# Kernel optimization log

Measured on AMD Instinct MI355X. Metric: run time of the kernel, lower is better.

Reference implementation:

```python
import jax, jax.numpy as jnp
import numpy as np

DIM = 20
N = 200000
E = 6400000
ITERATIONS = 3


def setup_inputs() -> dict:
    key = jax.random.key(0)
    ks = jax.random.split(key, 20)
    inp = {
        "h": jax.random.normal(ks[0], (N, DIM), dtype=jnp.float32),
        "node2depth": jax.random.randint(ks[1], (N,), 0, 5, dtype=jnp.int32),
        "edge_src": jax.random.randint(ks[2], (E,), 0, N, dtype=jnp.int32),
        "edge_dst": jax.random.randint(ks[3], (E,), 0, N, dtype=jnp.int32),
    }
    # Six DIM x DIM Linear layers (weight stored [out,in] like torch, plus bias)
    scale = 1.0 / np.sqrt(DIM)
    names = ["Wz", "Uz", "Wr", "Ur", "Wh", "Uh"]
    for j, nm in enumerate(names):
        inp[nm + "_w"] = jax.random.uniform(ks[4 + 2 * j], (DIM, DIM), jnp.float32, -scale, scale)
        inp[nm + "_b"] = jax.random.uniform(ks[5 + 2 * j], (DIM,), jnp.float32, -scale, scale)
    return inp


def _linear(x, w, b):
    return x @ w.T + b


def reference(h, Wz_w, Wz_b, Uz_w, Uz_b, Wr_w, Wr_b, Ur_w, Ur_b,
              Wh_w, Wh_b, Uh_w, Uh_b, node2depth, edge_src, edge_dst):
    active = None
    for i in range(ITERATIONS):
        # active set shrinks as i grows (depth + i <= ITERATIONS)
        active = (node2depth + i) <= ITERATIONS  # [N] bool
        af = active.astype(h.dtype)
        # x[u] = sum over neighbors v of h[v], counting only active src AND active dst
        msg = h[edge_src] * af[edge_src][:, None]          # [E, DIM]
        x = jax.ops.segment_sum(msg, edge_dst, num_segments=N)  # [N, DIM]
        x = x * af[:, None]
        z = jax.nn.sigmoid(_linear(x, Wz_w, Wz_b) + _linear(h, Uz_w, Uz_b))
        r = jax.nn.sigmoid(_linear(x, Wr_w, Wr_b) + _linear(h, Ur_w, Ur_b))
        h_cand = jnp.tanh(_linear(x, Wh_w, Wh_b) + _linear(r * h, Uh_w, Uh_b))
        h_new = z * h + (1.0 - z) * h_cand
        # inactive nodes are dropped from the dict in the original; since the
        # active set only shrinks, keeping their old h is equivalent
        h = jnp.where(active[:, None], h_new, h)
    # original returns only nodes active at the last iteration; zero out the rest
    return jnp.where(active[:, None], h, jnp.zeros_like(h))
```

## Files before the change

kernel.cpp:

```cpp
#include <hip/hip_runtime.h>

#define DIM    20
#define NN     200000
#define EE     6400000
#define ITERS  3
#define BLOCK  256

#define NODES_PER_FINE   64
#define NFINE            3125
#define NCOARSE          98
#define FINE_PER_COARSE  32

#define TILE1            2048
#define IPT1             8

#define TILE             4096
#define IPT              16

#define CAP1             57344
#define NT2P             14
#define CAP2             2048
#define PIPT             8

#define XSTRIDE          21

typedef unsigned int u32;

__device__ __forceinline__ u32 pack_bf16x2(float a, float b) {
    u32 ua = __float_as_uint(a);
    u32 ub = __float_as_uint(b);
    ua = (ua + 0x7FFFu + ((ua >> 16) & 1u)) >> 16;
    ub = (ub + 0x7FFFu + ((ub >> 16) & 1u)) & 0xFFFF0000u;
    return ua | ub;
}

__global__ __launch_bounds__(BLOCK) void setup(const float* __restrict__ h,
                                               const int* __restrict__ depth,
                                               u32* __restrict__ hbA,
                                               u32* __restrict__ hbC,
                                               u32* __restrict__ CT,
                                               int* __restrict__ coarse_cursor,
                                               int* __restrict__ fine_cursor,
                                               int* __restrict__ gcur) {
    int g = blockIdx.x * BLOCK + threadIdx.x;
    if (g < NCOARSE) coarse_cursor[g] = g * CAP1;
    if (g < NFINE)   fine_cursor[g]   = g * CAP2;
    if (g == 0) *gcur = 0;
    if (g < NN / 8) {
        int4 a = *(const int4*)(depth + g * 8);
        int4 b = *(const int4*)(depth + g * 8 + 4);
        CT[g] = ((u32)a.x & 7u)        | (((u32)a.y & 7u) << 4)
              | (((u32)a.z & 7u) << 8) | (((u32)a.w & 7u) << 12)
              | (((u32)b.x & 7u) << 16)| (((u32)b.y & 7u) << 20)
              | (((u32)b.z & 7u) << 24)| (((u32)b.w & 7u) << 28);
    }
    int node = g >> 3, s = g & 7;
    if (depth[node] > ITERS) return;
    float2 f = *(const float2*)(h + (size_t)node * DIM + s * 2);
    hbA[(size_t)node * 8 + s] = pack_bf16x2(f.x, f.y);
    if (s < 2) {
        float2 fc = *(const float2*)(h + (size_t)node * DIM + 16 + s * 2);
        hbC[(size_t)node * 2 + s] = pack_bf16x2(fc.x, fc.y);
    }
}

__global__ __launch_bounds__(BLOCK) void p1_split(const int* __restrict__ esrc,
                                                  const int* __restrict__ edst,
                                                  const u32* __restrict__ CT,
                                                  int* __restrict__ coarse_cursor,
                                                  u32* __restrict__ buf1) {
    __shared__ u32 hist[NCOARSE];
    __shared__ u32 lbase[NCOARSE];
    __shared__ u32 gbase[NCOARSE];
    __shared__ u32 lout[TILE1];
    int tid = threadIdx.x;
    int start = blockIdx.x * TILE1;
    if (tid < NCOARSE) hist[tid] = 0;
    __syncthreads();

    int4 d4[2], s4[2];
    #pragma unroll
    for (int q = 0; q < 2; ++q) {
        int e4 = start + (q * BLOCK + tid) * 4;
        d4[q] = *(const int4*)(edst + e4);
        s4[q] = *(const int4*)(esrc + e4);
    }
    int dd[IPT1], ss[IPT1];
    dd[0]=d4[0].x; dd[1]=d4[0].y; dd[2]=d4[0].z; dd[3]=d4[0].w;
    dd[4]=d4[1].x; dd[5]=d4[1].y; dd[6]=d4[1].z; dd[7]=d4[1].w;
    ss[0]=s4[0].x; ss[1]=s4[0].y; ss[2]=s4[0].z; ss[3]=s4[0].w;
    ss[4]=s4[1].x; ss[5]=s4[1].y; ss[6]=s4[1].z; ss[7]=s4[1].w;

    u32 cls[IPT1];
    #pragma unroll
    for (int k = 0; k < IPT1; ++k)
        cls[k] = (CT[(u32)ss[k] >> 3] >> (((u32)ss[k] & 7u) << 2)) & 7u;
    asm volatile("" :: "v"(cls[0]), "v"(cls[1]), "v"(cls[2]), "v"(cls[3]),
                       "v"(cls[4]), "v"(cls[5]), "v"(cls[6]), "v"(cls[7]));

    u32 rank[IPT1];
    #pragma unroll
    for (int k = 0; k < IPT1; ++k)
        if (cls[k] <= 3u) rank[k] = atomicAdd(&hist[(u32)dd[k] >> 11], 1u);
    __syncthreads();

    if (tid < 64) {
        u32 a = hist[tid];
        u32 b = (tid + 64 < NCOARSE) ? hist[tid + 64] : 0u;
        u32 ia = a, ib = b;
        #pragma unroll
        for (int off = 1; off < 64; off <<= 1) {
            u32 ta = (u32)__shfl_up((int)ia, off, 64);
            u32 tb = (u32)__shfl_up((int)ib, off, 64);
            if (tid >= off) { ia += ta; ib += tb; }
        }
        u32 totA = (u32)__shfl((int)ia, 63, 64);
        lbase[tid] = ia - a;
        if (tid + 64 < NCOARSE) lbase[tid + 64] = totA + ib - b;
    }
    __syncthreads();
    if (tid < NCOARSE) {
        u32 cq = hist[tid];
        gbase[tid] = cq ? (u32)atomicAdd((u32*)&coarse_cursor[tid], cq) : 0u;
    }
    #pragma unroll
    for (int k = 0; k < IPT1; ++k)
        if (cls[k] <= 3u)
            lout[lbase[(u32)dd[k] >> 11] + rank[k]] =
                ((u32)dd[k] & 2047u) | ((u32)ss[k] << 11) | (cls[k] << 29);
    __syncthreads();
    int wid = tid >> 6, lane = tid & 63;
    for (int b = wid; b < NCOARSE; b += 4) {
        u32 cq = hist[b], lb = lbase[b], gb = gbase[b];
        for (u32 i = lane; i < cq; i += 64)
            buf1[gb + i] = lout[lb + i];
    }
}

__global__ __launch_bounds__(BLOCK) void p2_split(const u32* __restrict__ buf1,
                                                  const int* __restrict__ coarse_cursor,
                                                  int* __restrict__ fine_cursor,
                                                  u32* __restrict__ buf2) {
    int bid = blockIdx.x;
    int c = bid / NT2P, t = bid - c * NT2P;
    int base  = c * CAP1;
    int end   = coarse_cursor[c];
    int start = base + t * TILE;
    if (start >= end) return;

    __shared__ u32 hist[FINE_PER_COARSE];
    __shared__ u32 lbase[FINE_PER_COARSE];
    __shared__ u32 gbase[FINE_PER_COARSE];
    __shared__ u32 lout[TILE];
    int tid = threadIdx.x;
    if (tid < FINE_PER_COARSE) hist[tid] = 0;
    __syncthreads();

    u32 w[IPT];
    #pragma unroll
    for (int q = 0; q < 4; ++q) {
        int i4 = start + (q * BLOCK + tid) * 4;
        if (i4 + 3 < end) {
            uint4 v = *(const uint4*)(buf1 + i4);
            w[q * 4 + 0] = v.x; w[q * 4 + 1] = v.y;
            w[q * 4 + 2] = v.z; w[q * 4 + 3] = v.w;
        } else {
            #pragma unroll
            for (int j = 0; j < 4; ++j) {
                int i = i4 + j;
                w[q * 4 + j] = (i < end) ? buf1[i] : 0xFFFFFFFFu;
            }
        }
    }
    u32 rank[IPT];
    #pragma unroll
    for (int k = 0; k < IPT; ++k)
        if (w[k] != 0xFFFFFFFFu)
            rank[k] = atomicAdd(&hist[(w[k] & 2047u) >> 6], 1u);
    __syncthreads();

    if (tid < 32) {
        u32 a = hist[tid], ia = a;
        #pragma unroll
        for (int off = 1; off < 32; off <<= 1) {
            u32 ta = (u32)__shfl_up((int)ia, off, 32);
            if (tid >= off) ia += ta;
        }
        lbase[tid] = ia - a;
        int f = c * FINE_PER_COARSE + tid;
        gbase[tid] = a ? (u32)atomicAdd((u32*)&fine_cursor[f], a) : 0u;
    }
    __syncthreads();
    #pragma unroll
    for (int k = 0; k < IPT; ++k)
        if (w[k] != 0xFFFFFFFFu)
            lout[lbase[(w[k] & 2047u) >> 6] + rank[k]] = (w[k] & 63u) | ((w[k] >> 11) << 6);
    __syncthreads();
    int wid = tid >> 6, lane = tid & 63;
    for (int b = wid; b < FINE_PER_COARSE; b += 4) {
        u32 cq = hist[b], lb = lbase[b], gb = gbase[b];
        for (u32 i = lane; i < cq; i += 64)
            buf2[gb + i] = lout[lb + i];
    }
}


__device__ __forceinline__ float bl(u32 w) { return __uint_as_float(w << 16); }
__device__ __forceinline__ float bh(u32 w) { return __uint_as_float(w & 0xFFFF0000u); }

__device__ __forceinline__ void acc_half(float* xa, float* xc, uint4 a, u32 c) {
    xa[0]+=bl(a.x); xa[1]+=bh(a.x);
    xa[2]+=bl(a.y); xa[3]+=bh(a.y);
    xa[4]+=bl(a.z); xa[5]+=bh(a.z);
    xa[6]+=bl(a.w); xa[7]+=bh(a.w);
    xc[0]+=bl(c);   xc[1]+=bh(c);
}

__device__ __forceinline__ float fast_sigmoid(float t) {
    return 1.0f / (1.0f + __expf(-t));
}
__device__ __forceinline__ float fast_tanh(float t) {
    t = fminf(fmaxf(t, -15.0f), 15.0f);
    float e2 = __expf(2.0f * t);
    return (e2 - 1.0f) / (e2 + 1.0f);
}

__device__ __forceinline__ void gru_body(
    int u, int tid, const float* xl,
    const float* __restrict__ h_in, float* __restrict__ h_out,
    u32* __restrict__ hbA_out, u32* __restrict__ hbC_out,
    int du, int limNext, int isFinal,
    const float* __restrict__ Wz, const float* __restrict__ bWz,
    const float* __restrict__ Uz, const float* __restrict__ bUz,
    const float* __restrict__ Wr, const float* __restrict__ bWr,
    const float* __restrict__ Ur, const float* __restrict__ bUr,
    const float* __restrict__ Wh, const float* __restrict__ bWh,
    const float* __restrict__ Uh, const float* __restrict__ bUh)
{
    float x[DIM], h[DIM];
    #pragma unroll
    for (int k = 0; k < DIM; ++k) x[k] = xl[tid * XSTRIDE + k];
    {
        const float4* hv = (const float4*)(h_in + (size_t)u * DIM);
        float4 a0 = hv[0], a1 = hv[1], a2 = hv[2], a3 = hv[3], a4 = hv[4];
        h[0]=a0.x; h[1]=a0.y; h[2]=a0.z; h[3]=a0.w;
        h[4]=a1.x; h[5]=a1.y; h[6]=a1.z; h[7]=a1.w;
        h[8]=a2.x; h[9]=a2.y; h[10]=a2.z; h[11]=a2.w;
        h[12]=a3.x; h[13]=a3.y; h[14]=a3.z; h[15]=a3.w;
        h[16]=a4.x; h[17]=a4.y; h[18]=a4.z; h[19]=a4.w;
    }

    float z[DIM], rh[DIM];
    #pragma unroll
    for (int j = 0; j < DIM; ++j) {
        float sz = bWz[j] + bUz[j];
        float sr = bWr[j] + bUr[j];
        #pragma unroll
        for (int k = 0; k < DIM; ++k) {
            sz += x[k] * Wz[j * DIM + k];
            sz += h[k] * Uz[j * DIM + k];
            sr += x[k] * Wr[j * DIM + k];
            sr += h[k] * Ur[j * DIM + k];
        }
        z[j]  = fast_sigmoid(sz);
        rh[j] = fast_sigmoid(sr) * h[j];
    }

    float o[DIM];
    #pragma unroll
    for (int j = 0; j < DIM; ++j) {
        float sh = bWh[j] + bUh[j];
        #pragma unroll
        for (int k = 0; k < DIM; ++k) {
            sh += x[k]  * Wh[j * DIM + k];
            sh += rh[k] * Uh[j * DIM + k];
        }
        float hc = fast_tanh(sh);
        o[j] = z[j] * h[j] + (1.0f - z[j]) * hc;
    }

    {
        float4* o4 = (float4*)(h_out + (size_t)u * DIM);
        o4[0] = make_float4(o[0],  o[1],  o[2],  o[3]);
        o4[1] = make_float4(o[4],  o[5],  o[6],  o[7]);
        o4[2] = make_float4(o[8],  o[9],  o[10], o[11]);
        o4[3] = make_float4(o[12], o[13], o[14], o[15]);
        o4[4] = make_float4(o[16], o[17], o[18], o[19]);
    }
    if (!isFinal && du <= limNext) {
        u32* rowA = hbA_out + (size_t)u * 8;
        uint4 wA0 = make_uint4(pack_bf16x2(o[0], o[1]),   pack_bf16x2(o[2], o[3]),
                               pack_bf16x2(o[4], o[5]),   pack_bf16x2(o[6], o[7]));
        uint4 wA1 = make_uint4(pack_bf16x2(o[8], o[9]),   pack_bf16x2(o[10], o[11]),
                               pack_bf16x2(o[12], o[13]), pack_bf16x2(o[14], o[15]));
        *(uint4*)rowA       = wA0;
        *(uint4*)(rowA + 4) = wA1;
        *(uint2*)(hbC_out + (size_t)u * 2) =
            make_uint2(pack_bf16x2(o[16], o[17]), pack_bf16x2(o[18], o[19]));
    }
}

__global__ __launch_bounds__(BLOCK) void pb_gru(
    const u32* __restrict__ buf2, const int* __restrict__ fine_cursor,
    int* __restrict__ gcur,
    int* __restrict__ ptr, u32* __restrict__ cnt3, u32* __restrict__ ssrc,
    const u32* __restrict__ hbA_in, const u32* __restrict__ hbC_in,
    u32* __restrict__ hbA_out, u32* __restrict__ hbC_out,
    const float* __restrict__ h_in, float* __restrict__ h_out,
    const int* __restrict__ depth,
    const float* __restrict__ Wz, const float* __restrict__ bWz,
    const float* __restrict__ Uz, const float* __restrict__ bUz,
    const float* __restrict__ Wr, const float* __restrict__ bWr,
    const float* __restrict__ Ur, const float* __restrict__ bUr,
    const float* __restrict__ Wh, const float* __restrict__ bWh,
    const float* __restrict__ Uh, const float* __restrict__ bUh)
{
    __shared__ u32 hist[512];
    __shared__ u32 ebase[512];
    __shared__ u32 lout[CAP2];
    __shared__ u32 wsum[4];
    __shared__ int slo;
    __shared__ float xl[64 * XSTRIDE];
    int tid = threadIdx.x;
    int f = blockIdx.x;
    int base = f * CAP2;
    int end  = fine_cursor[f];
    int cnt  = end - base;
    hist[tid] = 0; hist[tid + 256] = 0;
    __syncthreads();

    u32 w[PIPT];
    #pragma unroll
    for (int q = 0; q < 2; ++q) {
        int i4 = base + (q * BLOCK + tid) * 4;
        if (i4 + 3 < end) {
            uint4 v = *(const uint4*)(buf2 + i4);
            w[q * 4 + 0] = v.x; w[q * 4 + 1] = v.y;
            w[q * 4 + 2] = v.z; w[q * 4 + 3] = v.w;
        } else {
            #pragma unroll
            for (int j = 0; j < 4; ++j) {
                int i = i4 + j;
                w[q * 4 + j] = (i < end) ? buf2[i] : 0xFFFFFFFFu;
            }
        }
    }
    u32 key[PIPT], rank[PIPT];
    #pragma unroll
    for (int k = 0; k < PIPT; ++k) {
        if (w[k] != 0xFFFFFFFFu) {
            u32 cls = (w[k] >> 24) & 7u;
            key[k]  = (w[k] & 63u) * 8u + cls;
            rank[k] = atomicAdd(&hist[key[k]], 1u);
        }
    }
    if (tid == 0) slo = atomicAdd(gcur, cnt);
    __syncthreads();
    {
        u32 s0 = hist[2 * tid], s1 = hist[2 * tid + 1];
        u32 s = s0 + s1;
        int lane = tid & 63, wid = tid >> 6;
        u32 incl = s;
        #pragma unroll
        for (int off = 1; off < 64; off <<= 1) {
            u32 t = __shfl_up((int)incl, off, 64);
            if (lane >= off) incl += t;
        }
        if (lane == 63) wsum[wid] = incl;
        __syncthreads();
        u32 woff = 0;
        for (int w2 = 0; w2 < wid; ++w2) woff += wsum[w2];
        u32 excl = woff + incl - s;
        ebase[2 * tid]     = excl;
        ebase[2 * tid + 1] = excl + s0;
    }
    __syncthreads();
    int lo = slo;
    if (tid < NODES_PER_FINE) {
        u32 base0 = ebase[tid * 8];
        u32 cc1 = ebase[tid * 8 + 2] - base0;
        u32 cc2 = ebase[tid * 8 + 3] - base0;
        u32 cc3 = ebase[tid * 8 + 4] - base0;
        int u = f * NODES_PER_FINE + tid;
        ptr[u]  = lo + (int)base0;
        cnt3[u] = cc1 | (cc2 << 10) | (cc3 << 20);
    }
    #pragma unroll
    for (int k = 0; k < PIPT; ++k) {
        if (w[k] != 0xFFFFFFFFu) lout[ebase[key[k]] + rank[k]] = (w[k] >> 6) & 0x3FFFFu;
    }
    __syncthreads();
    for (int j = tid; j < cnt; j += BLOCK) ssrc[lo + j] = lout[j];

    int t = tid & 7, team = tid >> 3;
    int r = t >> 1, q = t & 1;
    #pragma unroll
    for (int rep = 0; rep < 2; ++rep) {
        int nl = team + rep * 32;
        int u = f * NODES_PER_FINE + nl;
        if (depth[u] <= ITERS) {
            int b0 = (int)ebase[nl * 8];
            int d  = (int)(ebase[nl * 8 + 4] - ebase[nl * 8]);

            float xa[8], xc[2];
            #pragma unroll
            for (int k = 0; k < 8; ++k) xa[k] = 0.0f;
            xc[0] = 0.0f; xc[1] = 0.0f;

            int e = r;
            for (; e + 12 < d; e += 16) {
                u32 p0 = lout[b0 + e];
                u32 p1 = lout[b0 + e + 4];
                u32 p2 = lout[b0 + e + 8];
                u32 p3 = lout[b0 + e + 12];
                uint4 a0 = *(const uint4*)(hbA_in + (size_t)p0 * 8 + q * 4);
                uint4 a1 = *(const uint4*)(hbA_in + (size_t)p1 * 8 + q * 4);
                uint4 a2 = *(const uint4*)(hbA_in + (size_t)p2 * 8 + q * 4);
                uint4 a3 = *(const uint4*)(hbA_in + (size_t)p3 * 8 + q * 4);
                u32 cc0 = hbC_in[(size_t)p0 * 2 + q];
                u32 cc1 = hbC_in[(size_t)p1 * 2 + q];
                u32 cc2 = hbC_in[(size_t)p2 * 2 + q];
                u32 cc3 = hbC_in[(size_t)p3 * 2 + q];
                acc_half(xa, xc, a0, cc0);
                acc_half(xa, xc, a1, cc1);
                acc_half(xa, xc, a2, cc2);
                acc_half(xa, xc, a3, cc3);
            }
            for (; e + 4 < d; e += 8) {
                u32 p0 = lout[b0 + e];
                u32 p1 = lout[b0 + e + 4];
                uint4 a0 = *(const uint4*)(hbA_in + (size_t)p0 * 8 + q * 4);
                uint4 a1 = *(const uint4*)(hbA_in + (size_t)p1 * 8 + q * 4);
                u32 cc0 = hbC_in[(size_t)p0 * 2 + q];
                u32 cc1 = hbC_in[(size_t)p1 * 2 + q];
                acc_half(xa, xc, a0, cc0);
                acc_half(xa, xc, a1, cc1);
            }
            if (e < d) {
                u32 p0 = lout[b0 + e];
                uint4 a0 = *(const uint4*)(hbA_in + (size_t)p0 * 8 + q * 4);
                u32 cc0 = hbC_in[(size_t)p0 * 2 + q];
                acc_half(xa, xc, a0, cc0);
            }
            #pragma unroll
            for (int k = 0; k < 8; ++k) {
                xa[k] += __shfl_xor(xa[k], 2, 64);
                xa[k] += __shfl_xor(xa[k], 4, 64);
            }
            xc[0] += __shfl_xor(xc[0], 2, 64); xc[0] += __shfl_xor(xc[0], 4, 64);
            xc[1] += __shfl_xor(xc[1], 2, 64); xc[1] += __shfl_xor(xc[1], 4, 64);

            float* xr = xl + nl * XSTRIDE;
            if (t == 0) {
                #pragma unroll
                for (int k = 0; k < 8; ++k) xr[k] = xa[k];
                xr[16] = xc[0]; xr[17] = xc[1];
            } else if (t == 1) {
                #pragma unroll
                for (int k = 0; k < 8; ++k) xr[8 + k] = xa[k];
                xr[18] = xc[0]; xr[19] = xc[1];
            }
        }
    }
    __syncthreads();
    if (tid >= 64) return;

    int u = f * NODES_PER_FINE + tid;
    int du = depth[u];
    if (du > ITERS) return;
    gru_body(u, tid, xl, h_in, h_out, hbA_out, hbC_out, du, 2, 0,
             Wz, bWz, Uz, bUz, Wr, bWr, Ur, bUr, Wh, bWh, Uh, bUh);
}


__global__ __launch_bounds__(BLOCK) void grnn_iter(
    const u32* __restrict__ hbA_in, const u32* __restrict__ hbC_in,
    u32* __restrict__ hbA_out, u32* __restrict__ hbC_out,
    const float* __restrict__ h_in, float* __restrict__ h_out,
    const int* __restrict__ depth, const int* __restrict__ ptr,
    const u32* __restrict__ cnt3, const u32* __restrict__ ssrc,
    const float* __restrict__ Wz, const float* __restrict__ bWz,
    const float* __restrict__ Uz, const float* __restrict__ bUz,
    const float* __restrict__ Wr, const float* __restrict__ bWr,
    const float* __restrict__ Ur, const float* __restrict__ bUr,
    const float* __restrict__ Wh, const float* __restrict__ bWh,
    const float* __restrict__ Uh, const float* __restrict__ bUh,
    int lim, int limNext, int shift, int isFinal)
{
    __shared__ float xl[64 * XSTRIDE];
    int tid = threadIdx.x;
    int t = tid & 7, team = tid >> 3;
    int r = t >> 1, q = t & 1;

    #pragma unroll
    for (int rep = 0; rep < 2; ++rep) {
        int nl = team + rep * 32;
        int u = blockIdx.x * 64 + nl;
        if (depth[u] <= lim) {
            int p = ptr[u];
            int d = (int)((cnt3[u] >> shift) & 1023u);

            float xa[8], xc[2];
            #pragma unroll
            for (int k = 0; k < 8; ++k) xa[k] = 0.0f;
            xc[0] = 0.0f; xc[1] = 0.0f;

            int e = r;
            for (; e + 12 < d; e += 16) {
                u32 p0 = ssrc[p + e];
                u32 p1 = ssrc[p + e + 4];
                u32 p2 = ssrc[p + e + 8];
                u32 p3 = ssrc[p + e + 12];
                uint4 a0 = *(const uint4*)(hbA_in + (size_t)p0 * 8 + q * 4);
                uint4 a1 = *(const uint4*)(hbA_in + (size_t)p1 * 8 + q * 4);
                uint4 a2 = *(const uint4*)(hbA_in + (size_t)p2 * 8 + q * 4);
                uint4 a3 = *(const uint4*)(hbA_in + (size_t)p3 * 8 + q * 4);
                u32 cc0 = hbC_in[(size_t)p0 * 2 + q];
                u32 cc1 = hbC_in[(size_t)p1 * 2 + q];
                u32 cc2 = hbC_in[(size_t)p2 * 2 + q];
                u32 cc3 = hbC_in[(size_t)p3 * 2 + q];
                acc_half(xa, xc, a0, cc0);
                acc_half(xa, xc, a1, cc1);
                acc_half(xa, xc, a2, cc2);
                acc_half(xa, xc, a3, cc3);
            }
            for (; e + 4 < d; e += 8) {
                u32 p0 = ssrc[p + e];
                u32 p1 = ssrc[p + e + 4];
                uint4 a0 = *(const uint4*)(hbA_in + (size_t)p0 * 8 + q * 4);
                uint4 a1 = *(const uint4*)(hbA_in + (size_t)p1 * 8 + q * 4);
                u32 cc0 = hbC_in[(size_t)p0 * 2 + q];
                u32 cc1 = hbC_in[(size_t)p1 * 2 + q];
                acc_half(xa, xc, a0, cc0);
                acc_half(xa, xc, a1, cc1);
            }
            if (e < d) {
                u32 p0 = ssrc[p + e];
                uint4 a0 = *(const uint4*)(hbA_in + (size_t)p0 * 8 + q * 4);
                u32 cc0 = hbC_in[(size_t)p0 * 2 + q];
                acc_half(xa, xc, a0, cc0);
            }
            #pragma unroll
            for (int k = 0; k < 8; ++k) {
                xa[k] += __shfl_xor(xa[k], 2, 64);
                xa[k] += __shfl_xor(xa[k], 4, 64);
            }
            xc[0] += __shfl_xor(xc[0], 2, 64); xc[0] += __shfl_xor(xc[0], 4, 64);
            xc[1] += __shfl_xor(xc[1], 2, 64); xc[1] += __shfl_xor(xc[1], 4, 64);

            float* xr = xl + nl * XSTRIDE;
            if (t == 0) {
                #pragma unroll
                for (int k = 0; k < 8; ++k) xr[k] = xa[k];
                xr[16] = xc[0]; xr[17] = xc[1];
            } else if (t == 1) {
                #pragma unroll
                for (int k = 0; k < 8; ++k) xr[8 + k] = xa[k];
                xr[18] = xc[0]; xr[19] = xc[1];
            }
        }
    }
    __syncthreads();
    if (tid >= 64) return;

    int u = blockIdx.x * 64 + tid;
    int du = depth[u];
    if (du > lim) {
        if (isFinal) {
            float4 z4 = make_float4(0.f, 0.f, 0.f, 0.f);
            float4* o4 = (float4*)(h_out + (size_t)u * DIM);
            #pragma unroll
            for (int qq = 0; qq < 5; ++qq) o4[qq] = z4;
        }
        return;
    }
    gru_body(u, tid, xl, h_in, h_out, hbA_out, hbC_out, du, limNext, isFinal,
             Wz, bWz, Uz, bUz, Wr, bWr, Ur, bUr, Wh, bWh, Uh, bUh);
}


extern "C" void kernel_launch(void* const* d_in, const int* in_sizes, int n_in,
                              void* d_out, int out_size, void* d_ws, size_t ws_size,
                              hipStream_t stream) {
    const float* h0    = (const float*)d_in[0];
    const int*   depth = (const int*)d_in[1];
    const int*   esrc  = (const int*)d_in[2];
    const int*   edst  = (const int*)d_in[3];
    const float* Wz  = (const float*)d_in[4];  const float* bWz = (const float*)d_in[5];
    const float* Uz  = (const float*)d_in[6];  const float* bUz = (const float*)d_in[7];
    const float* Wr  = (const float*)d_in[8];  const float* bWr = (const float*)d_in[9];
    const float* Ur  = (const float*)d_in[10]; const float* bUr = (const float*)d_in[11];
    const float* Wh  = (const float*)d_in[12]; const float* bWh = (const float*)d_in[13];
    const float* Uh  = (const float*)d_in[14]; const float* bUh = (const float*)d_in[15];
    float* out = (float*)d_out;

    int* W = (int*)d_ws;
    u32*  CT            = (u32*)(W + 0);
    int*  gcur          = W + 25024;
    int*  coarse_cursor = W + 25088;
    int*  fine_cursor   = W + 25216;
    int*  ptr           = W + 28416;
    u32*  cnt3          = (u32*)(W + 228416);
    u32*  buf1          = (u32*)(W + 428416);
    u32*  buf2          = buf1 + (size_t)NCOARSE * CAP1;
    float* h1           = (float*)(buf2 + (size_t)NFINE * CAP2);
    u32*  hbA0          = (u32*)(h1 + (size_t)NN * DIM);
    u32*  hbC0          = hbA0 + (size_t)NN * 8;
    u32*  hbA1          = hbC0 + (size_t)NN * 2;
    u32*  hbC1          = hbA1 + (size_t)NN * 8;
    u32*  ssrc          = buf1;

    setup   <<<(NN * 8) / BLOCK, BLOCK, 0, stream>>>(h0, depth, hbA0, hbC0, CT,
                                                     coarse_cursor, fine_cursor, gcur);
    p1_split<<<EE / TILE1, BLOCK, 0, stream>>>(esrc, edst, CT, coarse_cursor, buf1);
    p2_split<<<NCOARSE * NT2P, BLOCK, 0, stream>>>(buf1, coarse_cursor, fine_cursor, buf2);

    pb_gru  <<<NFINE, BLOCK, 0, stream>>>(buf2, fine_cursor, gcur, ptr, cnt3, ssrc,
        hbA0, hbC0, hbA1, hbC1, h0, h1, depth,
        Wz, bWz, Uz, bUz, Wr, bWr, Ur, bUr, Wh, bWh, Uh, bUh);

    grnn_iter<<<NN / 64, BLOCK, 0, stream>>>(hbA1, hbC1, hbA0, hbC0, h1, h1,
        depth, ptr, cnt3, ssrc,
        Wz, bWz, Uz, bUz, Wr, bWr, Ur, bUr, Wh, bWh, Uh, bUh, 2, 1, 10, 0);
    grnn_iter<<<NN / 64, BLOCK, 0, stream>>>(hbA0, hbC0, hbA1, hbC1, h1, out,
        depth, ptr, cnt3, ssrc,
        Wz, bWz, Uz, bUz, Wr, bWr, Ur, bUr, Wh, bWh, Uh, bUh, 1, 0, 0, 1);
}
```

Baseline: 485.1 us.

## Sort fused-kernel gather edges by source-id bucket for locality

In the fused partition+GRU kernel, a second LDS histogram and counting sort orders each destination node's edges by a 2-bit bucket of the source id (bits 22-23 of the packed word). The two node-teams per thread group then interleave their gathers chunk by chunk, so concurrent loads across the block hit a narrower range of source rows and get better L2/MALL locality. The cost is extra LDS (another 2048-entry buffer plus a 256-entry histogram), more LDS atomics, an extra scan with barriers, and a lower unroll depth in the gather loop. The existing lout/ssrc output used by later iterations is unchanged.

```diff
diff --git a/kernel.cpp b/kernel.cpp
--- a/kernel.cpp
+++ b/kernel.cpp
@@ -317,7 +317,10 @@
 {
     __shared__ u32 hist[512];
     __shared__ u32 ebase[512];
+    __shared__ u32 hist2[256];
+    __shared__ u32 ebase2[256];
     __shared__ u32 lout[CAP2];
+    __shared__ u32 lout2[CAP2];
     __shared__ u32 wsum[4];
     __shared__ int slo;
     __shared__ float xl[64 * XSTRIDE];
@@ -326,7 +329,7 @@
     int base = f * CAP2;
     int end  = fine_cursor[f];
     int cnt  = end - base;
-    hist[tid] = 0; hist[tid + 256] = 0;
+    hist[tid] = 0; hist[tid + 256] = 0; hist2[tid] = 0;
     __syncthreads();
 
     u32 w[PIPT];
@@ -345,13 +348,15 @@
             }
         }
     }
-    u32 key[PIPT], rank[PIPT];
+    u32 key[PIPT], rank[PIPT], rank2[PIPT];
     #pragma unroll
     for (int k = 0; k < PIPT; ++k) {
         if (w[k] != 0xFFFFFFFFu) {
             u32 cls = (w[k] >> 24) & 7u;
             key[k]  = (w[k] & 63u) * 8u + cls;
             rank[k] = atomicAdd(&hist[key[k]], 1u);
+            u32 key2 = (w[k] & 63u) * 4u + ((w[k] >> 22) & 3u);
+            rank2[k] = atomicAdd(&hist2[key2], 1u);
         }
     }
     if (tid == 0) slo = atomicAdd(gcur, cnt);
@@ -373,6 +378,22 @@
         u32 excl = woff + incl - s;
         ebase[2 * tid]     = excl;
         ebase[2 * tid + 1] = excl + s0;
+    }
+    __syncthreads();
+    {
+        u32 a = hist2[tid];
+        int lane = tid & 63, wid = tid >> 6;
+        u32 incl = a;
+        #pragma unroll
+        for (int off = 1; off < 64; off <<= 1) {
+            u32 t = __shfl_up((int)incl, off, 64);
+            if (lane >= off) incl += t;
+        }
+        if (lane == 63) wsum[wid] = incl;
+        __syncthreads();
+        u32 woff = 0;
+        for (int w2 = 0; w2 < wid; ++w2) woff += wsum[w2];
+        ebase2[tid] = woff + incl - a;
     }
     __syncthreads();
     int lo = slo;
@@ -387,79 +408,110 @@
     }
     #pragma unroll
     for (int k = 0; k < PIPT; ++k) {
-        if (w[k] != 0xFFFFFFFFu) lout[ebase[key[k]] + rank[k]] = (w[k] >> 6) & 0x3FFFFu;
+        if (w[k] != 0xFFFFFFFFu) {
+            u32 id = (w[k] >> 6) & 0x3FFFFu;
+            lout[ebase[key[k]] + rank[k]] = id;
+            u32 key2 = (w[k] & 63u) * 4u + ((w[k] >> 22) & 3u);
+            lout2[ebase2[key2] + rank2[k]] = id;
+        }
     }
     __syncthreads();
     for (int j = tid; j < cnt; j += BLOCK) ssrc[lo + j] = lout[j];
 
     int t = tid & 7, team = tid >> 3;
     int r = t >> 1, q = t & 1;
-    #pragma unroll
-    for (int rep = 0; rep < 2; ++rep) {
-        int nl = team + rep * 32;
-        int u = f * NODES_PER_FINE + nl;
-        if (depth[u] <= ITERS) {
-            int b0 = (int)ebase[nl * 8];
-            int d  = (int)(ebase[nl * 8 + 4] - ebase[nl * 8]);
-
-            float xa[8], xc[2];
-            #pragma unroll
-            for (int k = 0; k < 8; ++k) xa[k] = 0.0f;
-            xc[0] = 0.0f; xc[1] = 0.0f;
-
+    int u0 = f * NODES_PER_FINE + team;
+    int u1 = u0 + 32;
+    bool a0ok = depth[u0] <= ITERS;
+    bool a1ok = depth[u1] <= ITERS;
+    float xa0[8], xc0[2], xa1[8], xc1[2];
+    #pragma unroll
+    for (int k = 0; k < 8; ++k) { xa0[k] = 0.0f; xa1[k] = 0.0f; }
+    xc0[0]=0.0f; xc0[1]=0.0f; xc1[0]=0.0f; xc1[1]=0.0f;
+
+    #pragma unroll
+    for (int chunk = 0; chunk < 4; ++chunk) {
+        if (a0ok) {
+            int bb = team * 4 + chunk;
+            int s0 = (int)ebase2[bb];
+            int sl = (int)hist2[bb];
             int e = r;
-            for (; e + 12 < d; e += 16) {
-                u32 p0 = lout[b0 + e];
-                u32 p1 = lout[b0 + e + 4];
-                u32 p2 = lout[b0 + e + 8];
-                u32 p3 = lout[b0 + e + 12];
-                uint4 a0 = *(const uint4*)(hbA_in + (size_t)p0 * 8 + q * 4);
-                uint4 a1 = *(const uint4*)(hbA_in + (size_t)p1 * 8 + q * 4);
-                uint4 a2 = *(const uint4*)(hbA_in + (size_t)p2 * 8 + q * 4);
-                uint4 a3 = *(const uint4*)(hbA_in + (size_t)p3 * 8 + q * 4);
-                u32 cc0 = hbC_in[(size_t)p0 * 2 + q];
-                u32 cc1 = hbC_in[(size_t)p1 * 2 + q];
-                u32 cc2 = hbC_in[(size_t)p2 * 2 + q];
-                u32 cc3 = hbC_in[(size_t)p3 * 2 + q];
-                acc_half(xa, xc, a0, cc0);
-                acc_half(xa, xc, a1, cc1);
-                acc_half(xa, xc, a2, cc2);
-                acc_half(xa, xc, a3, cc3);
-            }
-            for (; e + 4 < d; e += 8) {
-                u32 p0 = lout[b0 + e];
-                u32 p1 = lout[b0 + e + 4];
-                uint4 a0 = *(const uint4*)(hbA_in + (size_t)p0 * 8 + q * 4);
-                uint4 a1 = *(const uint4*)(hbA_in + (size_t)p1 * 8 + q * 4);
-                u32 cc0 = hbC_in[(size_t)p0 * 2 + q];
-                u32 cc1 = hbC_in[(size_t)p1 * 2 + q];
-                acc_half(xa, xc, a0, cc0);
-                acc_half(xa, xc, a1, cc1);
-            }
-            if (e < d) {
-                u32 p0 = lout[b0 + e];
-                uint4 a0 = *(const uint4*)(hbA_in + (size_t)p0 * 8 + q * 4);
-                u32 cc0 = hbC_in[(size_t)p0 * 2 + q];
-                acc_half(xa, xc, a0, cc0);
-            }
-            #pragma unroll
-            for (int k = 0; k < 8; ++k) {
-                xa[k] += __shfl_xor(xa[k], 2, 64);
-                xa[k] += __shfl_xor(xa[k], 4, 64);
-            }
-            xc[0] += __shfl_xor(xc[0], 2, 64); xc[0] += __shfl_xor(xc[0], 4, 64);
-            xc[1] += __shfl_xor(xc[1], 2, 64); xc[1] += __shfl_xor(xc[1], 4, 64);
-
-            float* xr = xl + nl * XSTRIDE;
-            if (t == 0) {
-                #pragma unroll
-                for (int k = 0; k < 8; ++k) xr[k] = xa[k];
-                xr[16] = xc[0]; xr[17] = xc[1];
-            } else if (t == 1) {
-                #pragma unroll
-                for (int k = 0; k < 8; ++k) xr[8 + k] = xa[k];
-                xr[18] = xc[0]; xr[19] = xc[1];
-            }
+            for (; e + 4 < sl; e += 8) {
+                u32 p0 = lout2[s0 + e];
+                u32 p1 = lout2[s0 + e + 4];
+                uint4 a0v = *(const uint4*)(hbA_in + (size_t)p0 * 8 + q * 4);
+                uint4 a1v = *(const uint4*)(hbA_in + (size_t)p1 * 8 + q * 4);
+                u32 c0v = hbC_in[(size_t)p0 * 2 + q];
+                u32 c1v = hbC_in[(size_t)p1 * 2 + q];
+                acc_half(xa0, xc0, a0v, c0v);
+                acc_half(xa0, xc0, a1v, c1v);
+            }
+            if (e < sl) {
+                u32 p0 = lout2[s0 + e];
+                uint4 a0v = *(const uint4*)(hbA_in + (size_t)p0 * 8 + q * 4);
+                u32 c0v = hbC_in[(size_t)p0 * 2 + q];
+                acc_half(xa0, xc0, a0v, c0v);
+            }
+        }
+        if (a1ok) {
+            int bb = (team + 32) * 4 + chunk;
+            int s0 = (int)ebase2[bb];
+            int sl = (int)hist2[bb];
+            int e = r;
+            for (; e + 4 < sl; e += 8) {
+                u32 p0 = lout2[s0 + e];
+                u32 p1 = lout2[s0 + e + 4];
+                uint4 a0v = *(const uint4*)(hbA_in + (size_t)p0 * 8 + q * 4);
+                uint4 a1v = *(const uint4*)(hbA_in + (size_t)p1 * 8 + q * 4);
+                u32 c0v = hbC_in[(size_t)p0 * 2 + q];
+                u32 c1v = hbC_in[(size_t)p1 * 2 + q];
+                acc_half(xa1, xc1, a0v, c0v);
+                acc_half(xa1, xc1, a1v, c1v);
+            }
+            if (e < sl) {
+                u32 p0 = lout2[s0 + e];
+                uint4 a0v = *(const uint4*)(hbA_in + (size_t)p0 * 8 + q * 4);
+                u32 c0v = hbC_in[(size_t)p0 * 2 + q];
+                acc_half(xa1, xc1, a0v, c0v);
+            }
+        }
+    }
+    if (a0ok) {
+        #pragma unroll
+        for (int k = 0; k < 8; ++k) {
+            xa0[k] += __shfl_xor(xa0[k], 2, 64);
+            xa0[k] += __shfl_xor(xa0[k], 4, 64);
+        }
+        xc0[0] += __shfl_xor(xc0[0], 2, 64); xc0[0] += __shfl_xor(xc0[0], 4, 64);
+        xc0[1] += __shfl_xor(xc0[1], 2, 64); xc0[1] += __shfl_xor(xc0[1], 4, 64);
+        float* xr = xl + team * XSTRIDE;
+        if (t == 0) {
+            #pragma unroll
+            for (int k = 0; k < 8; ++k) xr[k] = xa0[k];
+            xr[16] = xc0[0]; xr[17] = xc0[1];
+        } else if (t == 1) {
+            #pragma unroll
+            for (int k = 0; k < 8; ++k) xr[8 + k] = xa0[k];
+            xr[18] = xc0[0]; xr[19] = xc0[1];
+        }
+    }
+    if (a1ok) {
+        #pragma unroll
+        for (int k = 0; k < 8; ++k) {
+            xa1[k] += __shfl_xor(xa1[k], 2, 64);
+            xa1[k] += __shfl_xor(xa1[k], 4, 64);
+        }
+        xc1[0] += __shfl_xor(xc1[0], 2, 64); xc1[0] += __shfl_xor(xc1[0], 4, 64);
+        xc1[1] += __shfl_xor(xc1[1], 2, 64); xc1[1] += __shfl_xor(xc1[1], 4, 64);
+        float* xr = xl + (team + 32) * XSTRIDE;
+        if (t == 0) {
+            #pragma unroll
+            for (int k = 0; k < 8; ++k) xr[k] = xa1[k];
+            xr[16] = xc1[0]; xr[17] = xc1[1];
+        } else if (t == 1) {
+            #pragma unroll
+            for (int k = 0; k < 8; ++k) xr[8 + k] = xa1[k];
+            xr[18] = xc1[0]; xr[19] = xc1[1];
         }
     }
     __syncthreads();
```

Result: slower. 531.1 us (+9.5%).
